# Performance work log

Measured on AMD Instinct MI355X. Metric: run time of the kernel, lower is better.

Reference implementation:

```python
import jax, jax.numpy as jnp
import numpy as np

N_BASIS = 7      # n_weights_per_edge
DEGREE = 3       # cubic B-splines
LO, HI = -1.0, 1.0
# clamped/open-uniform knot vector of length N_BASIS + DEGREE + 1 = 11
_KNOTS = np.concatenate([np.full(DEGREE, LO), np.linspace(LO, HI, N_BASIS - DEGREE + 1), np.full(DEGREE, HI)]).astype(np.float32)


def bspline_basis(x):
    """Cox-de Boor cubic B-spline basis. x: [...] -> [..., N_BASIS]."""
    t = jnp.asarray(_KNOTS, dtype=x.dtype)
    xe = jnp.clip(x, LO, HI - 1e-6)[..., None]
    N = ((xe >= t[:-1]) & (xe < t[1:])).astype(x.dtype)  # [..., 10]
    for d in range(1, DEGREE + 1):
        ld = t[d:-1] - t[:-(d + 1)]
        rd = t[d + 1:] - t[1:-d]
        left = jnp.where(ld > 0, (xe - t[:-(d + 1)]) / jnp.where(ld > 0, ld, 1.0), 0.0) * N[..., :-1]
        right = jnp.where(rd > 0, (t[d + 1:] - xe) / jnp.where(rd > 0, rd, 1.0), 0.0) * N[..., 1:]
        N = left + right
    return N  # [..., 7]


def extract_patches(x, k=3):
    # x [B,C,H,W] -> [B,Ho,Wo,C*k*k], channel-major flatten matching region.flatten()
    B, C, H, W = x.shape
    Ho, Wo = H - k + 1, W - k + 1
    cols = [x[:, :, i:i + Ho, j:j + Wo] for i in range(k) for j in range(k)]  # k*k x [B,C,Ho,Wo]
    p = jnp.stack(cols, axis=2).reshape(B, C * k * k, Ho, Wo)
    return jnp.transpose(p, (0, 2, 3, 1))


def kan_conv(x, W):
    # W: [out_ch, C*k*k, N_BASIS]; out[b,o,i,j] = sum_e sum_k W[o,e,k]*B_k(patch[b,i,j,e])
    patches = extract_patches(x, 3)               # [B,Ho,Wo,E]
    bases = bspline_basis(patches)                 # [B,Ho,Wo,E,7]
    return jnp.einsum('bhwek,oek->bohw', bases, W)


def kan_dense(v, W):
    # v: [n_in], W: [n_out, n_in, 7]
    bases = bspline_basis(v)                       # [n_in,7]
    return jnp.einsum('ek,oek->o', bases, W)


def setup_inputs() -> dict:
    key = jax.random.key(0)
    k0, k1, k2, k3, k4 = jax.random.split(key, 5)
    H = W = 384
    n_in = (H - 4) * (W - 4)  # 144400
    u = lambda k, s: jax.random.uniform(k, s, jnp.float32, -1.0, 1.0)  # weights_range=[-1,1]
    return {
        'x': jax.random.normal(k0, (1, 3, H, W), jnp.float32),
        'W1': u(k1, (2, 3 * 9, N_BASIS)),
        'W2': u(k2, (1, 2 * 9, N_BASIS)),
        'W3': u(k3, (32, n_in, N_BASIS)),
        'W4': u(k4, (10, 32, N_BASIS)),
    }


def reference(x, W1, W2, W3, W4):
    h = kan_conv(x, W1)     # [1,2,382,382]
    h = kan_conv(h, W2)     # [1,1,380,380]
    v = h.reshape(-1)       # flatten (batch==1)
    h1 = kan_dense(v, W3)   # [32]
    out = kan_dense(h1, W4) # [10]
    return out
```

## Files before the change

kernel.cpp:

```cpp
#include <hip/hip_runtime.h>

__device__ __forceinline__ void bspline7(float x, float B[7]) {
    constexpr float t[11] = {-1.f, -1.f, -1.f, -1.f, -0.5f, 0.f, 0.5f, 1.f, 1.f, 1.f, 1.f};
    float xe = fminf(fmaxf(x, -1.f), 0.999999f);
    float N[10];
#pragma unroll
    for (int i = 0; i < 10; ++i)
        N[i] = (xe >= t[i] && xe < t[i + 1]) ? 1.f : 0.f;
#pragma unroll
    for (int d = 1; d <= 3; ++d) {
#pragma unroll
        for (int i = 0; i + d < 10; ++i) {
            float ld = t[i + d] - t[i];
            float rd = t[i + d + 1] - t[i + 1];
            float left  = (ld > 0.f) ? (xe - t[i]) / ld * N[i] : 0.f;
            float right = (rd > 0.f) ? (t[i + d + 1] - xe) / rd * N[i + 1] : 0.f;
            N[i] = left + right;
        }
    }
#pragma unroll
    for (int k = 0; k < 7; ++k) B[k] = N[k];
}

#define H0 384
#define H1 382
#define H2 380
#define NX (3 * H0 * H0)
#define NP1 (H1 * H1)
#define NP2 (H2 * H2)
#define L_DENSE (NP2 * 7)
#define L4_DENSE (L_DENSE / 4)

__global__ __launch_bounds__(256) void k0_basis_x(const float* __restrict__ x,
                                                  float* __restrict__ Bx,
                                                  float* __restrict__ acc32) {
    int idx = blockIdx.x * blockDim.x + threadIdx.x;
    if (blockIdx.x == 0 && threadIdx.x < 32) acc32[threadIdx.x] = 0.f;
    if (idx >= NX) return;
    float B[7];
    bspline7(x[idx], B);
#pragma unroll
    for (int k = 0; k < 7; ++k) Bx[idx * 7 + k] = B[k];
}

__global__ __launch_bounds__(256) void k1_conv1(const float* __restrict__ Bx,
                                                const float* __restrict__ W1,
                                                float* __restrict__ Bh) {
    __shared__ float w[2 * 27 * 7];
    for (int i = threadIdx.x; i < 378; i += blockDim.x) w[i] = W1[i];
    __syncthreads();
    int p = blockIdx.x * blockDim.x + threadIdx.x;
    if (p >= NP1) return;
    int i = p / H1, j = p % H1;
    float acc0 = 0.f, acc1 = 0.f;
#pragma unroll
    for (int c = 0; c < 3; ++c)
#pragma unroll
        for (int di = 0; di < 3; ++di)
#pragma unroll
            for (int dj = 0; dj < 3; ++dj) {
                const float* b = &Bx[(((c * H0) + (i + di)) * H0 + (j + dj)) * 7];
                int e = c * 9 + di * 3 + dj;
                const float* w0 = &w[e * 7];
                const float* w1 = &w[189 + e * 7];
#pragma unroll
                for (int k = 0; k < 7; ++k) {
                    float bv = b[k];
                    acc0 += bv * w0[k];
                    acc1 += bv * w1[k];
                }
            }
    float B0[7], B1[7];
    bspline7(acc0, B0);
    bspline7(acc1, B1);
#pragma unroll
    for (int k = 0; k < 7; ++k) {
        Bh[(size_t)p * 7 + k] = B0[k];
        Bh[((size_t)NP1 + p) * 7 + k] = B1[k];
    }
}

__global__ __launch_bounds__(256) void k2_conv2(const float* __restrict__ Bh,
                                                const float* __restrict__ W2,
                                                float* __restrict__ Bv) {
    __shared__ float w[18 * 7];
    for (int i = threadIdx.x; i < 126; i += blockDim.x) w[i] = W2[i];
    __syncthreads();
    int p = blockIdx.x * blockDim.x + threadIdx.x;
    if (p >= NP2) return;
    int i = p / H2, j = p % H2;
    float acc = 0.f;
#pragma unroll
    for (int c = 0; c < 2; ++c)
#pragma unroll
        for (int di = 0; di < 3; ++di)
#pragma unroll
            for (int dj = 0; dj < 3; ++dj) {
                const float* b = &Bh[((size_t)c * NP1 + (i + di) * H1 + (j + dj)) * 7];
                const float* we = &w[(c * 9 + di * 3 + dj) * 7];
#pragma unroll
                for (int k = 0; k < 7; ++k) acc += b[k] * we[k];
            }
    float B[7];
    bspline7(acc, B);
#pragma unroll
    for (int k = 0; k < 7; ++k) Bv[p * 7 + k] = B[k];
}

__global__ __launch_bounds__(256) void k3_dense1(const float* __restrict__ W3,
                                                 const float* __restrict__ Bv,
                                                 float* __restrict__ acc32) {
    int o = blockIdx.y;
    const float4* w = (const float4*)(W3 + (size_t)o * L_DENSE);
    const float4* b = (const float4*)Bv;
    float s = 0.f;
    for (int f = blockIdx.x * blockDim.x + threadIdx.x; f < L4_DENSE;
         f += gridDim.x * blockDim.x) {
        float4 wv = w[f];
        float4 bv = b[f];
        s += wv.x * bv.x + wv.y * bv.y + wv.z * bv.z + wv.w * bv.w;
    }
#pragma unroll
    for (int off = 32; off > 0; off >>= 1) s += __shfl_down(s, off, 64);
    __shared__ float ws[4];
    int wave = threadIdx.x >> 6;
    if ((threadIdx.x & 63) == 0) ws[wave] = s;
    __syncthreads();
    if (threadIdx.x == 0) {
        float bs = ws[0] + ws[1] + ws[2] + ws[3];
        atomicAdd(&acc32[o], bs);
    }
}

__global__ void k4_dense2(const float* __restrict__ acc32, const float* __restrict__ W4,
                          float* __restrict__ out) {
    int o = threadIdx.x;
    if (o >= 10) return;
    float s = 0.f;
    for (int e = 0; e < 32; ++e) {
        float B[7];
        bspline7(acc32[e], B);
#pragma unroll
        for (int k = 0; k < 7; ++k) s += B[k] * W4[(o * 32 + e) * 7 + k];
    }
    out[o] = s;
}

extern "C" void kernel_launch(void* const* d_in, const int* in_sizes, int n_in,
                              void* d_out, int out_size, void* d_ws, size_t ws_size,
                              hipStream_t stream) {
    const float* x  = (const float*)d_in[0];
    const float* W1 = (const float*)d_in[1];
    const float* W2 = (const float*)d_in[2];
    const float* W3 = (const float*)d_in[3];
    const float* W4 = (const float*)d_in[4];
    float* out = (float*)d_out;

    char* ws = (char*)d_ws;
    float* acc32 = (float*)ws;
    float* Bx = (float*)(ws + 128);
    float* Bh = (float*)(ws + 128 + 12386304);
    float* Bv = (float*)(ws + 128 + 12386304 + 8171744);

    k0_basis_x<<<(NX + 255) / 256, 256, 0, stream>>>(x, Bx, acc32);
    k1_conv1<<<(NP1 + 255) / 256, 256, 0, stream>>>(Bx, W1, Bh);
    k2_conv2<<<(NP2 + 255) / 256, 256, 0, stream>>>(Bh, W2, Bv);
    k3_dense1<<<dim3(64, 32), 256, 0, stream>>>(W3, Bv, acc32);
    k4_dense2<<<1, 64, 0, stream>>>(acc32, W4, out);
}
```

Baseline: 235.5 us.

## Fuse basis, conv1 and conv2 into one tiled kernel using shared memory

Replaces the three separate kernels (input basis, conv1, conv2) with one kernel that works on 16x16 output tiles. The input-basis and conv1-basis halos are computed into LDS, which removes the large global intermediates Bx and Bh. The cost is recomputing halo regions and using about 65KB of LDS per block, which limits occupancy. The W3 stream in the dense kernel also switches to nontemporal loads.

```diff
diff --git a/kernel.cpp b/kernel.cpp
--- a/kernel.cpp
+++ b/kernel.cpp
@@ -1,4 +1,6 @@
 #include <hip/hip_runtime.h>
+
+typedef float f32x4 __attribute__((ext_vector_type(4)));
 
 __device__ __forceinline__ void bspline7(float x, float B[7]) {
     constexpr float t[11] = {-1.f, -1.f, -1.f, -1.f, -0.5f, 0.f, 0.5f, 1.f, 1.f, 1.f, 1.f};
@@ -25,115 +27,123 @@
 #define H0 384
 #define H1 382
 #define H2 380
-#define NX (3 * H0 * H0)
-#define NP1 (H1 * H1)
 #define NP2 (H2 * H2)
 #define L_DENSE (NP2 * 7)
 #define L4_DENSE (L_DENSE / 4)
+#define TILE 16
+#define HTILE 18
+#define XTILE 20
 
-__global__ __launch_bounds__(256) void k0_basis_x(const float* __restrict__ x,
-                                                  float* __restrict__ Bx,
-                                                  float* __restrict__ acc32) {
-    int idx = blockIdx.x * blockDim.x + threadIdx.x;
-    if (blockIdx.x == 0 && threadIdx.x < 32) acc32[threadIdx.x] = 0.f;
-    if (idx >= NX) return;
-    float B[7];
-    bspline7(x[idx], B);
+__global__ __launch_bounds__(256) void k_fused(const float* __restrict__ x,
+                                               const float* __restrict__ W1,
+                                               const float* __restrict__ W2,
+                                               float* __restrict__ Bv,
+                                               float* __restrict__ acc32) {
+    __shared__ float w1[378];
+    __shared__ float w2[126];
+    __shared__ float bx[3 * XTILE * XTILE * 7];
+    __shared__ float bh[2 * HTILE * HTILE * 7];
+
+    const int tid = threadIdx.x;
+    const int i0 = blockIdx.y * TILE;
+    const int j0 = blockIdx.x * TILE;
+
+    if (blockIdx.x == 0 && blockIdx.y == 0 && tid < 32) acc32[tid] = 0.f;
+
+    for (int i = tid; i < 378; i += 256) w1[i] = W1[i];
+    for (int i = tid; i < 126; i += 256) w2[i] = W2[i];
+
+    for (int t = tid; t < 3 * XTILE * XTILE; t += 256) {
+        int c = t / (XTILE * XTILE);
+        int r = t % (XTILE * XTILE);
+        int ii = r / XTILE, jj = r % XTILE;
+        int gi = i0 + ii, gj = j0 + jj;
+        float xv = (gi < H0 && gj < H0) ? x[(c * H0 + gi) * H0 + gj] : 0.f;
+        float B[7];
+        bspline7(xv, B);
 #pragma unroll
-    for (int k = 0; k < 7; ++k) Bx[idx * 7 + k] = B[k];
-}
+        for (int k = 0; k < 7; ++k) bx[t * 7 + k] = B[k];
+    }
+    __syncthreads();
 
-__global__ __launch_bounds__(256) void k1_conv1(const float* __restrict__ Bx,
-                                                const float* __restrict__ W1,
-                                                float* __restrict__ Bh) {
-    __shared__ float w[2 * 27 * 7];
-    for (int i = threadIdx.x; i < 378; i += blockDim.x) w[i] = W1[i];
+    for (int t = tid; t < HTILE * HTILE; t += 256) {
+        int i1 = t / HTILE, j1 = t % HTILE;
+        float acc0 = 0.f, acc1 = 0.f;
+#pragma unroll
+        for (int c = 0; c < 3; ++c)
+#pragma unroll
+            for (int di = 0; di < 3; ++di)
+#pragma unroll
+                for (int dj = 0; dj < 3; ++dj) {
+                    const float* b = &bx[(((c * XTILE) + (i1 + di)) * XTILE + (j1 + dj)) * 7];
+                    int e = c * 9 + di * 3 + dj;
+                    const float* u0 = &w1[e * 7];
+                    const float* u1 = &w1[189 + e * 7];
+#pragma unroll
+                    for (int k = 0; k < 7; ++k) {
+                        float bvv = b[k];
+                        acc0 += bvv * u0[k];
+                        acc1 += bvv * u1[k];
+                    }
+                }
+        float B0[7], B1[7];
+        bspline7(acc0, B0);
+        bspline7(acc1, B1);
+#pragma unroll
+        for (int k = 0; k < 7; ++k) {
+            bh[t * 7 + k] = B0[k];
+            bh[(HTILE * HTILE + t) * 7 + k] = B1[k];
+        }
+    }
     __syncthreads();
-    int p = blockIdx.x * blockDim.x + threadIdx.x;
-    if (p >= NP1) return;
-    int i = p / H1, j = p % H1;
-    float acc0 = 0.f, acc1 = 0.f;
+
+    int li = tid / TILE, lj = tid % TILE;
+    int gi2 = i0 + li, gj2 = j0 + lj;
+    if (gi2 < H2 && gj2 < H2) {
+        float acc = 0.f;
 #pragma unroll
-    for (int c = 0; c < 3; ++c)
+        for (int c = 0; c < 2; ++c)
 #pragma unroll
-        for (int di = 0; di < 3; ++di)
+            for (int di = 0; di < 3; ++di)
 #pragma unroll
-            for (int dj = 0; dj < 3; ++dj) {
-                const float* b = &Bx[(((c * H0) + (i + di)) * H0 + (j + dj)) * 7];
-                int e = c * 9 + di * 3 + dj;
-                const float* w0 = &w[e * 7];
-                const float* w1 = &w[189 + e * 7];
+                for (int dj = 0; dj < 3; ++dj) {
+                    const float* b = &bh[((c * HTILE + (li + di)) * HTILE + (lj + dj)) * 7];
+                    const float* u = &w2[(c * 9 + di * 3 + dj) * 7];
 #pragma unroll
-                for (int k = 0; k < 7; ++k) {
-                    float bv = b[k];
-                    acc0 += bv * w0[k];
-                    acc1 += bv * w1[k];
+                    for (int k = 0; k < 7; ++k) acc += b[k] * u[k];
                 }
-            }
-    float B0[7], B1[7];
-    bspline7(acc0, B0);
-    bspline7(acc1, B1);
+        float B[7];
+        bspline7(acc, B);
+        size_t p = (size_t)gi2 * H2 + gj2;
 #pragma unroll
-    for (int k = 0; k < 7; ++k) {
-        Bh[(size_t)p * 7 + k] = B0[k];
-        Bh[((size_t)NP1 + p) * 7 + k] = B1[k];
+        for (int k = 0; k < 7; ++k) Bv[p * 7 + k] = B[k];
     }
 }
 
-__global__ __launch_bounds__(256) void k2_conv2(const float* __restrict__ Bh,
-                                                const float* __restrict__ W2,
-                                                float* __restrict__ Bv) {
-    __shared__ float w[18 * 7];
-    for (int i = threadIdx.x; i < 126; i += blockDim.x) w[i] = W2[i];
-    __syncthreads();
-    int p = blockIdx.x * blockDim.x + threadIdx.x;
-    if (p >= NP2) return;
-    int i = p / H2, j = p % H2;
-    float acc = 0.f;
-#pragma unroll
-    for (int c = 0; c < 2; ++c)
-#pragma unroll
-        for (int di = 0; di < 3; ++di)
-#pragma unroll
-            for (int dj = 0; dj < 3; ++dj) {
-                const float* b = &Bh[((size_t)c * NP1 + (i + di) * H1 + (j + dj)) * 7];
-                const float* we = &w[(c * 9 + di * 3 + dj) * 7];
-#pragma unroll
-                for (int k = 0; k < 7; ++k) acc += b[k] * we[k];
-            }
-    float B[7];
-    bspline7(acc, B);
-#pragma unroll
-    for (int k = 0; k < 7; ++k) Bv[p * 7 + k] = B[k];
-}
-
-__global__ __launch_bounds__(256) void k3_dense1(const float* __restrict__ W3,
-                                                 const float* __restrict__ Bv,
-                                                 float* __restrict__ acc32) {
+__global__ __launch_bounds__(256) void k_dense1(const float* __restrict__ W3,
+                                                const float* __restrict__ Bv,
+                                                float* __restrict__ acc32) {
     int o = blockIdx.y;
-    const float4* w = (const float4*)(W3 + (size_t)o * L_DENSE);
-    const float4* b = (const float4*)Bv;
+    const f32x4* w = (const f32x4*)(W3 + (size_t)o * L_DENSE);
+    const f32x4* b = (const f32x4*)Bv;
     float s = 0.f;
     for (int f = blockIdx.x * blockDim.x + threadIdx.x; f < L4_DENSE;
          f += gridDim.x * blockDim.x) {
-        float4 wv = w[f];
-        float4 bv = b[f];
+        f32x4 wv = __builtin_nontemporal_load(&w[f]);
+        f32x4 bv = b[f];
         s += wv.x * bv.x + wv.y * bv.y + wv.z * bv.z + wv.w * bv.w;
     }
 #pragma unroll
     for (int off = 32; off > 0; off >>= 1) s += __shfl_down(s, off, 64);
-    __shared__ float ws[4];
-    int wave = threadIdx.x >> 6;
-    if ((threadIdx.x & 63) == 0) ws[wave] = s;
+    __shared__ float red[4];
+    if ((threadIdx.x & 63) == 0) red[threadIdx.x >> 6] = s;
     __syncthreads();
-    if (threadIdx.x == 0) {
-        float bs = ws[0] + ws[1] + ws[2] + ws[3];
-        atomicAdd(&acc32[o], bs);
-    }
+    if (threadIdx.x == 0)
+        atomicAdd(&acc32[o], red[0] + red[1] + red[2] + red[3]);
 }
 
-__global__ void k4_dense2(const float* __restrict__ acc32, const float* __restrict__ W4,
-                          float* __restrict__ out) {
+__global__ void k_dense2(const float* __restrict__ acc32, const float* __restrict__ W4,
+                         float* __restrict__ out) {
     int o = threadIdx.x;
     if (o >= 10) return;
     float s = 0.f;
@@ -158,13 +168,10 @@
 
     char* ws = (char*)d_ws;
     float* acc32 = (float*)ws;
-    float* Bx = (float*)(ws + 128);
-    float* Bh = (float*)(ws + 128 + 12386304);
-    float* Bv = (float*)(ws + 128 + 12386304 + 8171744);
+    float* Bv = (float*)(ws + 128);
 
-    k0_basis_x<<<(NX + 255) / 256, 256, 0, stream>>>(x, Bx, acc32);
-    k1_conv1<<<(NP1 + 255) / 256, 256, 0, stream>>>(Bx, W1, Bh);
-    k2_conv2<<<(NP2 + 255) / 256, 256, 0, stream>>>(Bh, W2, Bv);
-    k3_dense1<<<dim3(64, 32), 256, 0, stream>>>(W3, Bv, acc32);
-    k4_dense2<<<1, 64, 0, stream>>>(acc32, W4, out);
+    dim3 gfuse((H2 + TILE - 1) / TILE, (H2 + TILE - 1) / TILE);
+    k_fused<<<gfuse, 256, 0, stream>>>(x, W1, W2, Bv, acc32);
+    k_dense1<<<dim3(64, 32), 256, 0, stream>>>(W3, Bv, acc32);
+    k_dense2<<<1, 64, 0, stream>>>(acc32, W4, out);
 }
```

Result: slower. 258.1 us (+9.6%).
